# Optimization experiments

Hardware: AMD Instinct MI355X
Metric: run time of the kernel (lower is better)

Reference implementation:

```python
import jax, jax.numpy as jnp
import numpy as np

EPS = 1e-12  # matches torch F.normalize eps


def _l2norm(t):
    n = jnp.linalg.norm(t, axis=-1, keepdims=True)
    return t / jnp.maximum(n, EPS)


def setup_inputs() -> dict:
    key = jax.random.key(0)
    ks = jax.random.split(key, 10)
    B, N, C = 2, 2048, 384
    nH, hd = 12, 32
    inp = {
        "x": jax.random.normal(ks[0], (B, N, C), jnp.float32),
        "q_w": jax.random.normal(ks[1], (C, C), jnp.float32) * 0.02,
        "q_b": jax.random.normal(ks[2], (C,), jnp.float32) * 0.02,
        "kv_w": jax.random.normal(ks[3], (2 * C, C), jnp.float32) * 0.02,
        "kv_b": jax.random.normal(ks[4], (2 * C,), jnp.float32) * 0.02,
        "query_embedding": jax.random.normal(ks[5], (nH, 1, hd), jnp.float32) * 0.02,
        # init of temperature in torch: log(exp(1/0.24) - 1)
        "temperature": jnp.full((nH, 1, 1), float(np.log(np.exp(1.0 / 0.24) - 1.0)), jnp.float32),
        "pos_bias": jax.random.normal(ks[7], (nH, N), jnp.float32) * 0.0004,
        "proj_w": jax.random.normal(ks[8], (C, C), jnp.float32) * 0.02,
        "proj_b": jax.random.normal(ks[9], (C,), jnp.float32) * 0.02,
        "D": 8, "H": 16, "W": 16,
    }
    return inp


def reference(x, q_w, q_b, kv_w, kv_b, query_embedding, temperature, pos_bias, proj_w, proj_b, D, H, W):
    B, N, C = x.shape
    nH, hd = query_embedding.shape[0], query_embedding.shape[2]
    assert N == D * H * W
    # q projection -> [B, nH, N, hd], cosine-normalized
    q = (x @ q_w.T + q_b).reshape(B, N, nH, hd).transpose(0, 2, 1, 3)
    q = _l2norm(q)
    # additive query embedding, softplus temperature, seq-length (log N) scale
    scale = jax.nn.softplus(temperature) * jnp.float32(np.log(N))  # [nH,1,1]
    q = (q + query_embedding[None]) * scale[None]
    # kv projection
    kv = x @ kv_w.T + kv_b  # [B, N, 2C]
    k, v = kv[..., :C], kv[..., C:]
    k = _l2norm(k.reshape(B, N, nH, hd).transpose(0, 2, 1, 3))
    v = v.reshape(B, N, nH, hd).transpose(0, 2, 1, 3)
    # scores with per-head learned positional bias over keys
    attn = jnp.einsum("bhqd,bhkd->bhqk", q, k) + pos_bias[None, :, None, :]
    attn = jax.nn.softmax(attn, axis=-1)
    out = jnp.einsum("bhqk,bhkd->bhqd", attn, v)
    out = out.transpose(0, 2, 1, 3).reshape(B, N, C)
    return out @ proj_w.T + proj_b
```

## Files before the change

kernel.cpp:

```cpp
#include <hip/hip_runtime.h>

#define LOG2E 1.4426950408889634f

typedef __bf16 bf16x8 __attribute__((ext_vector_type(8)));
typedef short s16x4 __attribute__((ext_vector_type(4)));
typedef float f32x4 __attribute__((ext_vector_type(4)));

#define BB 2
#define NN 2048
#define CC 384
#define NH 12
#define HD 32
#define MROWS (BB * NN)

__device__ __forceinline__ unsigned short f2bf(float f) {
  __bf16 h = (__bf16)f;
  return __builtin_bit_cast(unsigned short, h);
}

__device__ __forceinline__ bf16x8 ldg_bf8(const unsigned short* p) {
  uint4 v = *reinterpret_cast<const uint4*>(p);
  return __builtin_bit_cast(bf16x8, v);
}

__device__ __forceinline__ float fexp2(float x) {
#if __has_builtin(__builtin_amdgcn_exp2f)
  return __builtin_amdgcn_exp2f(x);
#else
  return exp2f(x);
#endif
}

__device__ __forceinline__ s16x4 pack_bf4(float a, float b, float c, float d) {
#if __has_builtin(__builtin_amdgcn_cvt_pk_bf16_f32)
  auto lo = __builtin_amdgcn_cvt_pk_bf16_f32(a, b);
  auto hi = __builtin_amdgcn_cvt_pk_bf16_f32(c, d);
  uint2 u = {__builtin_bit_cast(unsigned int, lo),
             __builtin_bit_cast(unsigned int, hi)};
  return __builtin_bit_cast(s16x4, u);
#else
  s16x4 r = {(short)f2bf(a), (short)f2bf(b), (short)f2bf(c), (short)f2bf(d)};
  return r;
#endif
}

typedef __attribute__((address_space(1))) const void gas_void;
typedef __attribute__((address_space(3))) void las_void;
__device__ __forceinline__ void gload_lds16(const void* g, void* l) {
  __builtin_amdgcn_global_load_lds((gas_void*)(unsigned long long)g,
                                   (las_void*)(unsigned long long)l, 16, 0, 0);
}

__device__ __forceinline__ f32x4 mfma32(bf16x8 a, bf16x8 b, f32x4 c) {
  return __builtin_amdgcn_mfma_f32_16x16x32_bf16(a, b, c, 0, 0, 0);
}

__device__ __forceinline__ f32x4 mfma16(s16x4 a, s16x4 b, f32x4 c) {
#if defined(__HIP_DEVICE_COMPILE__)
#if __has_builtin(__builtin_amdgcn_mfma_f32_16x16x16bf16_1k)
  return __builtin_amdgcn_mfma_f32_16x16x16bf16_1k(a, b, c, 0, 0, 0);
#else
  asm volatile("v_mfma_f32_16x16x16_bf16 %0, %1, %2, %0"
               : "+v"(c) : "v"(a), "v"(b));
  return c;
#endif
#else
  return c;
#endif
}

__global__ __launch_bounds__(256) void prep_kernel(
    const float* __restrict__ x, const float* __restrict__ q_w,
    const float* __restrict__ kv_w, const float* __restrict__ proj_w,
    const float* __restrict__ pos_bias, unsigned short* __restrict__ xb,
    unsigned short* __restrict__ qwb, unsigned short* __restrict__ kvwb,
    unsigned short* __restrict__ pwb, float* __restrict__ bias2) {
  int i = blockIdx.x * 256 + threadIdx.x;
  if (i < 1572864) { xb[i] = f2bf(x[i]); return; }
  i -= 1572864;
  if (i < 147456) { qwb[i] = f2bf(q_w[i]); return; }
  i -= 147456;
  if (i < 294912) { kvwb[i] = f2bf(kv_w[i]); return; }
  i -= 294912;
  if (i < 147456) { pwb[i] = f2bf(proj_w[i]); return; }
  i -= 147456;
  bias2[i] = pos_bias[i] * LOG2E;
}

__global__ __launch_bounds__(256, 4) void gemm_qkv_norm_kernel(
    const unsigned short* __restrict__ xb, const unsigned short* __restrict__ qwb,
    const unsigned short* __restrict__ kvwb, const float* __restrict__ q_b,
    const float* __restrict__ kv_b, const float* __restrict__ qe,
    const float* __restrict__ temperature, unsigned short* __restrict__ Qs,
    unsigned short* __restrict__ Kn, unsigned short* __restrict__ VT) {
  __shared__ alignas(16) char smem[2][20480];
  int wave = threadIdx.x >> 6, lane = threadIdx.x & 63;
  int c = lane & 15, quad = lane >> 4;
  int h = blockIdx.y;
  int m0b = blockIdx.x * 64;
  int cid = wave * 64 + lane;

  auto stage = [&](int buf, int kk) {
    char* base = smem[buf];
#pragma unroll
    for (int j = 0; j < 2; ++j) {
      int chunk = j * 256 + cid;
      int row = chunk >> 3, e = chunk & 7;
      gload_lds16(xb + (long)(m0b + row) * CC + kk + e * 8,
                  base + j * 4096 + wave * 1024);
    }
#pragma unroll
    for (int j = 0; j < 3; ++j) {
      int chunk = j * 256 + cid;
      int row = chunk >> 3, e = chunk & 7;
      const unsigned short* src;
      if (row < 32)      src = qwb + (long)(h * 32 + row) * CC;
      else if (row < 64) src = kvwb + (long)(h * 32 + (row - 32)) * CC;
      else               src = kvwb + (long)(CC + h * 32 + (row - 64)) * CC;
      gload_lds16(src + kk + e * 8, base + 8192 + j * 4096 + wave * 1024);
    }
  };

  f32x4 acc[6] = {};
  auto compute = [&](int buf) {
    const char* base = smem[buf];
#pragma unroll
    for (int kh = 0; kh < 2; ++kh) {
      bf16x8 a = *(const bf16x8*)(base + (wave * 16 + c) * 128 + kh * 64 + quad * 16);
#pragma unroll
      for (int t = 0; t < 6; ++t) {
        bf16x8 b = *(const bf16x8*)(base + 8192 + (t * 16 + c) * 128 + kh * 64 + quad * 16);
        acc[t] = mfma32(a, b, acc[t]);
      }
    }
  };

  stage(0, 0);
#pragma unroll 1
  for (int s = 0; s < 6; ++s) {
    __syncthreads();
    if (s < 5) stage((s + 1) & 1, (s + 1) * 64);
    compute(s & 1);
  }

  int m0 = m0b + wave * 16;
  float qb0 = q_b[h * 32 + c], qb1 = q_b[h * 32 + 16 + c];
  float kb0 = kv_b[h * 32 + c], kb1 = kv_b[h * 32 + 16 + c];
  float vb0 = kv_b[CC + h * 32 + c], vb1 = kv_b[CC + h * 32 + 16 + c];
  float qe0 = qe[h * HD + c], qe1 = qe[h * HD + 16 + c];
  float sc = log1pf(expf(temperature[h])) * 11.0f;
  int b = m0 >> 11;
  int nb = (m0 & 2047) + quad * 4;
  int pair = b * NH + h;
  unsigned short* qsb = Qs + ((long)pair * NN + nb) * HD;
  unsigned short* knb = Kn + ((long)pair * NN + nb) * HD;
  ushort4 vp0, vp1;
#pragma unroll
  for (int r = 0; r < 4; ++r) {
    float q0 = acc[0][r] + qb0, q1 = acc[1][r] + qb1;
    float k0 = acc[2][r] + kb0, k1 = acc[3][r] + kb1;
    float v0 = acc[4][r] + vb0, v1 = acc[5][r] + vb1;
    float qs = q0 * q0 + q1 * q1, ks = k0 * k0 + k1 * k1;
#pragma unroll
    for (int off = 8; off; off >>= 1) {
      qs += __shfl_xor(qs, off);
      ks += __shfl_xor(ks, off);
    }
    float qi = 1.0f / fmaxf(sqrtf(qs), 1e-12f);
    float ki = 1.0f / fmaxf(sqrtf(ks), 1e-12f);
    qsb[r * HD + c] = f2bf((q0 * qi + qe0) * sc);
    qsb[r * HD + 16 + c] = f2bf((q1 * qi + qe1) * sc);
    knb[r * HD + c] = f2bf(k0 * ki);
    knb[r * HD + 16 + c] = f2bf(k1 * ki);
    ((unsigned short*)&vp0)[r] = f2bf(v0);
    ((unsigned short*)&vp1)[r] = f2bf(v1);
  }
  *reinterpret_cast<ushort4*>(VT + ((long)pair * HD + c) * NN + nb) = vp0;
  *reinterpret_cast<ushort4*>(VT + ((long)pair * HD + 16 + c) * NN + nb) = vp1;
}

__global__ __launch_bounds__(512, 4) void attn_kernel(
    const unsigned short* __restrict__ Qs, const unsigned short* __restrict__ Kn,
    const unsigned short* __restrict__ VT, const float* __restrict__ bias2,
    unsigned short* __restrict__ ao) {
  __shared__ alignas(16) char smem[2][2][16384];
  __shared__ alignas(16) char biasl[8192];
  int wave = threadIdx.x >> 6, lane = threadIdx.x & 63;
  int half = wave >> 2, sw = wave & 3;
  int c = lane & 15, quad = lane >> 4;
  int id = blockIdx.x;
  int xcd = id & 7, rr = id >> 3;
  int pair = (rr >> 5) * 8 + xcd;
  int qt = rr & 31;
  int h = pair % NH, b = pair / NH;
  const unsigned short* Qp = Qs + (long)pair * NN * HD;
  const char* Kg0 = (const char*)(Kn + (long)pair * NN * HD);
  const char* Vg0 = (const char*)(VT + (long)pair * HD * NN);
  const char* bp = (const char*)(bias2 + h * NN);
  int q0 = qt * 64 + sw * 16;
  bf16x8 qf = ldg_bf8(Qp + (long)(q0 + c) * HD + quad * 8);
  f32x4 o0 = {}, o1 = {};
  float rs = 0.f;

  const int koff = (c * 4 + quad) * 16;

  auto stage = [&](int buf, int i) {
    char* tb = smem[buf][half];
    long krow0 = half * 1024 + i * 128;
    const char* Kg = Kg0 + krow0 * (HD * 2);
    const char* Vg = Vg0 + krow0 * 2;
#pragma unroll
    for (int j = 0; j < 2; ++j) {
      int ck = sw * 2 + j;
      gload_lds16(Kg + ck * 1024 + koff, tb + ck * 1024);
      int chunk = ck * 64 + lane;
      int d = chunk >> 4, e = chunk & 15;
      int es = e ^ (d & 15);
      gload_lds16(Vg + (long)d * (NN * 2) + es * 16, tb + 8192 + ck * 1024);
    }
  };

  auto compute = [&](int buf, int i) {
    const char* kb = smem[buf][half] + lane * 16;
    const char* vb = smem[buf][half] + 8192;
    const char* bl = biasl + (half * 8 + i) * 512 + quad * 16;
#pragma unroll
    for (int t8 = 0; t8 < 8; ++t8) {
      bf16x8 kf = *(const bf16x8*)(kb + t8 * 1024);
      f32x4 bbv = *(const f32x4*)(bl + t8 * 64);
      f32x4 s = mfma32(kf, qf, bbv);
      float p0 = fexp2(s[0]);
      float p1 = fexp2(s[1]);
      float p2 = fexp2(s[2]);
      float p3 = fexp2(s[3]);
      rs += (p0 + p1) + (p2 + p3);
      s16x4 pf = pack_bf4(p0, p1, p2, p3);
      int vsw = (((t8 * 2 + (quad >> 1)) ^ c) * 16) + (quad & 1) * 8;
      s16x4 vlo = *(const s16x4*)(vb + c * 256 + vsw);
      s16x4 vhi = *(const s16x4*)(vb + (c + 16) * 256 + vsw);
      o0 = mfma16(vlo, pf, o0);
      o1 = mfma16(vhi, pf, o1);
    }
  };

  gload_lds16(bp + wave * 1024 + lane * 16, biasl + wave * 1024);
  stage(0, 0);
#pragma unroll 1
  for (int i = 0; i < 8; ++i) {
    __syncthreads();
    if (i < 7) stage((i + 1) & 1, i + 1);
    compute(i & 1, i);
  }

  rs += __shfl_xor(rs, 16);
  rs += __shfl_xor(rs, 32);

  __syncthreads();
  float* comb = (float*)&smem[0][0][0];
  if (half == 1) {
    float* p = comb + (sw * 64 + lane) * 9;
#pragma unroll
    for (int r = 0; r < 4; ++r) { p[r] = o0[r]; p[4 + r] = o1[r]; }
    p[8] = rs;
  }
  __syncthreads();
  if (half == 0) {
    const float* p = comb + (sw * 64 + lane) * 9;
#pragma unroll
    for (int r = 0; r < 4; ++r) { o0[r] += p[r]; o1[r] += p[4 + r]; }
    rs += p[8];
    float inv = 1.0f / rs;
    unsigned short* op = ao + (long)(b * NN + q0 + c) * CC + h * HD + quad * 4;
    ushort4 s0, s1;
#pragma unroll
    for (int r = 0; r < 4; ++r) {
      ((unsigned short*)&s0)[r] = f2bf(o0[r] * inv);
      ((unsigned short*)&s1)[r] = f2bf(o1[r] * inv);
    }
    *reinterpret_cast<ushort4*>(op) = s0;
    *reinterpret_cast<ushort4*>(op + 16) = s1;
  }
}

__global__ __launch_bounds__(256, 4) void proj_kernel(
    const unsigned short* __restrict__ ab, const unsigned short* __restrict__ pwb,
    const float* __restrict__ proj_b, float* __restrict__ out) {
  __shared__ alignas(16) char smem[2][16384];
  int wave = threadIdx.x >> 6, lane = threadIdx.x & 63;
  int c = lane & 15, quad = lane >> 4;
  int m0b = blockIdx.x * 64;
  int n0 = blockIdx.y * 64;
  int cid = wave * 64 + lane;

  auto stage = [&](int buf, int kk) {
    char* base = smem[buf];
#pragma unroll
    for (int j = 0; j < 2; ++j) {
      int chunk = j * 256 + cid;
      int row = chunk >> 3, e = chunk & 7;
      gload_lds16(ab + (long)(m0b + row) * CC + kk + e * 8,
                  base + j * 4096 + wave * 1024);
      gload_lds16(pwb + (long)(n0 + row) * CC + kk + e * 8,
                  base + 8192 + j * 4096 + wave * 1024);
    }
  };

  f32x4 acc[4] = {};
  auto compute = [&](int buf) {
    const char* base = smem[buf];
#pragma unroll
    for (int kh = 0; kh < 2; ++kh) {
      bf16x8 a = *(const bf16x8*)(base + (wave * 16 + c) * 128 + kh * 64 + quad * 16);
#pragma unroll
      for (int t = 0; t < 4; ++t) {
        bf16x8 b = *(const bf16x8*)(base + 8192 + (t * 16 + c) * 128 + kh * 64 + quad * 16);
        acc[t] = mfma32(a, b, acc[t]);
      }
    }
  };

  stage(0, 0);
#pragma unroll 1
  for (int s = 0; s < 6; ++s) {
    __syncthreads();
    if (s < 5) stage((s + 1) & 1, (s + 1) * 64);
    compute(s & 1);
  }

  int m0 = m0b + wave * 16;
#pragma unroll
  for (int t = 0; t < 4; ++t) {
    int o = n0 + t * 16 + c;
    float bv = proj_b[o];
#pragma unroll
    for (int r = 0; r < 4; ++r) {
      out[(long)(m0 + quad * 4 + r) * CC + o] = acc[t][r] + bv;
    }
  }
}

extern "C" void kernel_launch(void* const* d_in, const int* in_sizes, int n_in,
                              void* d_out, int out_size, void* d_ws, size_t ws_size,
                              hipStream_t stream) {
  const float* x = (const float*)d_in[0];
  const float* q_w = (const float*)d_in[1];
  const float* q_b = (const float*)d_in[2];
  const float* kv_w = (const float*)d_in[3];
  const float* kv_b = (const float*)d_in[4];
  const float* qe = (const float*)d_in[5];
  const float* temp = (const float*)d_in[6];
  const float* pos_bias = (const float*)d_in[7];
  const float* proj_w = (const float*)d_in[8];
  const float* proj_b = (const float*)d_in[9];
  float* out = (float*)d_out;

  char* ws = (char*)d_ws;
  unsigned short* xb = (unsigned short*)(ws + 0);
  unsigned short* qwb = (unsigned short*)(ws + 3145728);
  unsigned short* kvwb = (unsigned short*)(ws + 3440640);
  unsigned short* pwb = (unsigned short*)(ws + 4030464);
  unsigned short* Qs = (unsigned short*)(ws + 4325376);
  unsigned short* Kn = (unsigned short*)(ws + 7471104);
  unsigned short* VT = (unsigned short*)(ws + 10616832);
  unsigned short* ao = (unsigned short*)(ws + 13762560);
  float* bias2 = (float*)(ws + 16908288);

  prep_kernel<<<8544, 256, 0, stream>>>(x, q_w, kv_w, proj_w, pos_bias, xb, qwb,
                                        kvwb, pwb, bias2);
  gemm_qkv_norm_kernel<<<dim3(64, NH), 256, 0, stream>>>(xb, qwb, kvwb, q_b, kv_b,
                                                         qe, temp, Qs, Kn, VT);
  attn_kernel<<<768, 512, 0, stream>>>(Qs, Kn, VT, bias2, ao);
  proj_kernel<<<dim3(64, 6), 256, 0, stream>>>(ao, pwb, proj_b, out);
}
```

Before: 132.5 us.

## Drop split-K halves in attention; one 4-wave block walks all keys

The attention kernel previously used 8 waves per block, with two groups of 4 waves each covering half the keys and merging partial outputs through shared memory. Now each block has 4 waves that loop over all 16 key tiles, which removes the cross-half combine, its two barriers and half the LDS staging buffers. The cost is a longer serial loop per wave and fewer waves in flight per block. Shared memory per block drops, so more blocks may fit per CU.

```diff
diff --git a/kernel.cpp b/kernel.cpp
--- a/kernel.cpp
+++ b/kernel.cpp
@@ -179,14 +179,13 @@
   *reinterpret_cast<ushort4*>(VT + ((long)pair * HD + 16 + c) * NN + nb) = vp1;
 }
 
-__global__ __launch_bounds__(512, 4) void attn_kernel(
+__global__ __launch_bounds__(256, 4) void attn_kernel(
     const unsigned short* __restrict__ Qs, const unsigned short* __restrict__ Kn,
     const unsigned short* __restrict__ VT, const float* __restrict__ bias2,
     unsigned short* __restrict__ ao) {
-  __shared__ alignas(16) char smem[2][2][16384];
+  __shared__ alignas(16) char smem[2][16384];
   __shared__ alignas(16) char biasl[8192];
   int wave = threadIdx.x >> 6, lane = threadIdx.x & 63;
-  int half = wave >> 2, sw = wave & 3;
   int c = lane & 15, quad = lane >> 4;
   int id = blockIdx.x;
   int xcd = id & 7, rr = id >> 3;
@@ -197,7 +196,7 @@
   const char* Kg0 = (const char*)(Kn + (long)pair * NN * HD);
   const char* Vg0 = (const char*)(VT + (long)pair * HD * NN);
   const char* bp = (const char*)(bias2 + h * NN);
-  int q0 = qt * 64 + sw * 16;
+  int q0 = qt * 64 + wave * 16;
   bf16x8 qf = ldg_bf8(Qp + (long)(q0 + c) * HD + quad * 8);
   f32x4 o0 = {}, o1 = {};
   float rs = 0.f;
@@ -205,13 +204,13 @@
   const int koff = (c * 4 + quad) * 16;
 
   auto stage = [&](int buf, int i) {
-    char* tb = smem[buf][half];
-    long krow0 = half * 1024 + i * 128;
+    char* tb = smem[buf];
+    long krow0 = (long)i * 128;
     const char* Kg = Kg0 + krow0 * (HD * 2);
     const char* Vg = Vg0 + krow0 * 2;
 #pragma unroll
     for (int j = 0; j < 2; ++j) {
-      int ck = sw * 2 + j;
+      int ck = wave * 2 + j;
       gload_lds16(Kg + ck * 1024 + koff, tb + ck * 1024);
       int chunk = ck * 64 + lane;
       int d = chunk >> 4, e = chunk & 15;
@@ -221,9 +220,9 @@
   };
 
   auto compute = [&](int buf, int i) {
-    const char* kb = smem[buf][half] + lane * 16;
-    const char* vb = smem[buf][half] + 8192;
-    const char* bl = biasl + (half * 8 + i) * 512 + quad * 16;
+    const char* kb = smem[buf] + lane * 16;
+    const char* vb = smem[buf] + 8192;
+    const char* bl = biasl + i * 512 + quad * 16;
 #pragma unroll
     for (int t8 = 0; t8 < 8; ++t8) {
       bf16x8 kf = *(const bf16x8*)(kb + t8 * 1024);
@@ -243,43 +242,30 @@
     }
   };
 
-  gload_lds16(bp + wave * 1024 + lane * 16, biasl + wave * 1024);
+#pragma unroll
+  for (int j = 0; j < 2; ++j)
+    gload_lds16(bp + j * 4096 + wave * 1024 + lane * 16,
+                biasl + j * 4096 + wave * 1024);
   stage(0, 0);
 #pragma unroll 1
-  for (int i = 0; i < 8; ++i) {
+  for (int i = 0; i < 16; ++i) {
     __syncthreads();
-    if (i < 7) stage((i + 1) & 1, i + 1);
+    if (i < 15) stage((i + 1) & 1, i + 1);
     compute(i & 1, i);
   }
 
   rs += __shfl_xor(rs, 16);
   rs += __shfl_xor(rs, 32);
-
-  __syncthreads();
-  float* comb = (float*)&smem[0][0][0];
-  if (half == 1) {
-    float* p = comb + (sw * 64 + lane) * 9;
-#pragma unroll
-    for (int r = 0; r < 4; ++r) { p[r] = o0[r]; p[4 + r] = o1[r]; }
-    p[8] = rs;
-  }
-  __syncthreads();
-  if (half == 0) {
-    const float* p = comb + (sw * 64 + lane) * 9;
-#pragma unroll
-    for (int r = 0; r < 4; ++r) { o0[r] += p[r]; o1[r] += p[4 + r]; }
-    rs += p[8];
-    float inv = 1.0f / rs;
-    unsigned short* op = ao + (long)(b * NN + q0 + c) * CC + h * HD + quad * 4;
-    ushort4 s0, s1;
-#pragma unroll
-    for (int r = 0; r < 4; ++r) {
-      ((unsigned short*)&s0)[r] = f2bf(o0[r] * inv);
-      ((unsigned short*)&s1)[r] = f2bf(o1[r] * inv);
-    }
-    *reinterpret_cast<ushort4*>(op) = s0;
-    *reinterpret_cast<ushort4*>(op + 16) = s1;
-  }
+  float inv = 1.0f / rs;
+  unsigned short* op = ao + (long)(b * NN + q0 + c) * CC + h * HD + quad * 4;
+  ushort4 s0, s1;
+#pragma unroll
+  for (int r = 0; r < 4; ++r) {
+    ((unsigned short*)&s0)[r] = f2bf(o0[r] * inv);
+    ((unsigned short*)&s1)[r] = f2bf(o1[r] * inv);
+  }
+  *reinterpret_cast<ushort4*>(op) = s0;
+  *reinterpret_cast<ushort4*>(op + 16) = s1;
 }
 
 __global__ __launch_bounds__(256, 4) void proj_kernel(
@@ -369,6 +355,6 @@
                                         kvwb, pwb, bias2);
   gemm_qkv_norm_kernel<<<dim3(64, NH), 256, 0, stream>>>(xb, qwb, kvwb, q_b, kv_b,
                                                          qe, temp, Qs, Kn, VT);
-  attn_kernel<<<768, 512, 0, stream>>>(Qs, Kn, VT, bias2, ao);
+  attn_kernel<<<768, 256, 0, stream>>>(Qs, Kn, VT, bias2, ao);
   proj_kernel<<<dim3(64, 6), 256, 0, stream>>>(ao, pwb, proj_b, out);
 }
```

Result: no change. 132.9 us (+0.3%).
